# Kernel optimization log

Measured on AMD Instinct MI355X. Metric: run time of the kernel, lower is better.

The kernel has to match this reference:

```python
import jax, jax.numpy as jnp
import numpy as np

# dims: P patches, D=N_azi*N_ele directions, R=P*D radiances, E COO edges,
# T echogram samples, F rfft bins
P, D, R, E, T, NOBJ = 128, 128, 16384, 131072, 1024, 8
F = T // 2 + 1
SR, C_SOUND = 16000.0, 343.0
LOG_GAMMA = float(np.log(1e-3))   # fsm_gamma = 0.001
AIR = 1e-3                        # air absorption coefficient
BOUNCES = 4                       # truncated num_bounces


def setup_inputs():
    key = jax.random.key(0)
    ks = jax.random.split(key, 11)
    return {
        "source_pos": jax.random.normal(ks[0], (3,), jnp.float32) * 2.0,
        "receiver_pos": jax.random.normal(ks[1], (3,), jnp.float32) * 2.0,
        "absorption": jax.random.uniform(ks[2], (NOBJ,), jnp.float32, minval=0.05, maxval=0.6),
        "scattering": jax.random.uniform(ks[3], (NOBJ,), jnp.float32, minval=0.1, maxval=0.9),
        "gk_val": jax.random.uniform(ks[4], (E,), jnp.float32) * 0.1,            # form factors
        "local_kernel_basis": jax.random.uniform(ks[5], (2, D, D), jnp.float32) / D,  # [brdf,Dout,Din]
        "average_distance": jax.random.uniform(ks[6], (R,), jnp.float32) * 10.0 + 1.0,  # meters
        "radiance_pos": jax.random.normal(ks[7], (R, 3), jnp.float32) * 5.0,
        "gk_row": jax.random.randint(ks[8], (E,), 0, R),
        "gk_col": jax.random.randint(ks[9], (E,), 0, R),
        "object_ids": jax.random.randint(ks[10], (P,), 0, NOBJ),
    }


def _path_factor(dist):
    """Frequency-domain factor for a propagation path of length dist [N] -> [N,F].
    Combines fractional delay phase, FSM exponential window gamma^(tau_sec),
    and air absorption exp(-alpha*dist)."""
    freqs = jnp.arange(F, dtype=jnp.float32)
    tau = dist * (SR / C_SOUND)  # delay in samples
    phase = jnp.exp((-2j * np.pi / T) * tau[:, None] * freqs[None, :])
    decay = jnp.exp((LOG_GAMMA / C_SOUND - AIR) * dist)  # fsm + air, per path
    return phase * decay[:, None].astype(phase.dtype)


def reference(source_pos, receiver_pos, absorption, scattering, gk_val,
              local_kernel_basis, average_distance, radiance_pos,
              gk_row, gk_col, object_ids):
    # --- injection: source -> patch-direction radiance [R,F] ---
    d_src = jnp.linalg.norm(radiance_pos - source_pos[None, :], axis=-1)
    g_src = 1.0 / (d_src * d_src + 1e-3)
    rad = g_src[:, None] * _path_factor(d_src)  # complex [R,F]

    # --- BRDF-factorized local kernel: K[p] = sum_b c[b,p] * B[b] ---
    refl = 1.0 - absorption                                   # [NOBJ]
    coeff = jnp.stack([refl * scattering, refl * (1.0 - scattering)])  # [2,NOBJ]
    c_patch = coeff[:, object_ids]                            # [2,P]
    K = jnp.einsum('bp,bde->pde', c_patch, local_kernel_basis)  # [P,Dout,Din]

    prop = _path_factor(average_distance)  # per-radiance transport delay/decay [R,F]

    def bounce(r):
        r = r.reshape(P, D, F)
        r = jnp.einsum('pde,pef->pdf', K.astype(jnp.complex64), r)  # local direction mixing
        r = r.reshape(R, F) * prop
        # sparse COO global kernel: out[row] += val * r[col]
        return jax.ops.segment_sum(gk_val[:, None] * r[gk_col], gk_row, num_segments=R)

    total = rad
    r = rad
    for _ in range(BOUNCES):
        r = bounce(r)
        total = total + r

    # --- detection: patch-direction radiance -> receiver echogram ---
    d_rec = jnp.linalg.norm(radiance_pos - receiver_pos[None, :], axis=-1)
    w_rec = 1.0 / (d_rec * d_rec + 1e-3)
    echo_f = jnp.sum(w_rec[:, None] * _path_factor(d_rec) * total, axis=0)  # [F]

    # FSM correction: divide out the exponential window in time domain
    t = jnp.arange(T, dtype=jnp.float32) / SR
    fsm_window = jnp.exp(LOG_GAMMA * t)
    echogram = jnp.fft.irfft(echo_f, n=T) / fsm_window
    return echogram
```

## Files before the change

kernel.cpp:

```cpp
#include <hip/hip_runtime.h>
#include <math.h>

#define PP 128
#define DD 128
#define RR 16384
#define EE 131072
#define TT 1024
#define FF 513
#define FP 520
#define FPW 528
#define FPITCH 1056
#define NRB 1024
#define PSTRIDE 528
#define EPITCH 136

#define TAU_SCALE 46.64723032069971
#define KDECAY   -0.0211392282f
#define LOG_GAMMA -6.907755278982137f
#define TWO_PI    6.283185307179586

typedef __attribute__((ext_vector_type(8))) short bf16x8;
typedef __attribute__((ext_vector_type(4))) float f32x4;
typedef unsigned short u16;

__device__ __forceinline__ u16 f2bf(float x) {
    unsigned u = __float_as_uint(x);
    unsigned r = (u + 0x7fffu + ((u >> 16) & 1u)) >> 16;
    return (u16)r;
}
__device__ __forceinline__ float bf2f(u16 b) {
    return __uint_as_float(((unsigned)b) << 16);
}

__device__ __forceinline__ void pf_sincos(float tau, int f, float* s, float* c) {
    int ti = (int)tau;
    float tf = tau - (float)ti;
    int m = (ti * f) & 1023;
    float u = fmaf(tf, (float)f, (float)m);
    float ang = u * -0.006135923151542565f;
    __sincosf(ang, s, c);
}

__global__ void k_per_row(const float* __restrict__ rpos,
                          const float* __restrict__ spos,
                          const float* __restrict__ cpos,
                          const float* __restrict__ avg_dist,
                          float* __restrict__ per_row) {
    int r = blockIdx.x * blockDim.x + threadIdx.x;
    if (r >= RR) return;
    float x = rpos[3*r], y = rpos[3*r+1], z = rpos[3*r+2];

    float dx = x - spos[0], dy = y - spos[1], dz = z - spos[2];
    float ds = sqrtf(dx*dx + dy*dy + dz*dz);
    per_row[0*RR + r] = (1.0f/(ds*ds + 0.001f)) * expf(KDECAY * ds);
    per_row[1*RR + r] = ds * (float)TAU_SCALE;

    dx = x - cpos[0]; dy = y - cpos[1]; dz = z - cpos[2];
    float dr = sqrtf(dx*dx + dy*dy + dz*dz);
    per_row[2*RR + r] = (1.0f/(dr*dr + 0.001f)) * expf(KDECAY * dr);
    per_row[3*RR + r] = dr * (float)TAU_SCALE;

    float da = avg_dist[r];
    per_row[4*RR + r] = expf(KDECAY * da);
    per_row[5*RR + r] = da * (float)TAU_SCALE;
}

__global__ void k_build_K(const float* __restrict__ absorption,
                          const float* __restrict__ scattering,
                          const int* __restrict__ object_ids,
                          const float* __restrict__ basis,
                          float* __restrict__ Kmat) {
    int idx = blockIdx.x * 256 + threadIdx.x;
    int p  = idx >> 14;
    int de = idx & 16383;
    int obj = object_ids[p];
    float refl = 1.0f - absorption[obj];
    float sc   = scattering[obj];
    Kmat[idx] = refl*sc*basis[de] + refl*(1.0f - sc)*basis[16384 + de];
}

__global__ void k_count(const int* __restrict__ gk_row, int* __restrict__ counts) {
    int e = blockIdx.x * 256 + threadIdx.x;
    atomicAdd(&counts[gk_row[e]], 1);
}

__global__ __launch_bounds__(1024) void k_scan(const int* __restrict__ counts,
                                               int* __restrict__ row_start,
                                               int* __restrict__ cursor) {
    __shared__ int sh[1024];
    int tid = threadIdx.x;
    int base = tid * 16;
    int local[16];
    int sum = 0;
    #pragma unroll
    for (int j = 0; j < 16; j++) { local[j] = sum; sum += counts[base + j]; }
    sh[tid] = sum;
    __syncthreads();
    for (int off = 1; off < 1024; off <<= 1) {
        int v = (tid >= off) ? sh[tid - off] : 0;
        __syncthreads();
        sh[tid] += v;
        __syncthreads();
    }
    int chunk_excl = sh[tid] - sum;
    #pragma unroll
    for (int j = 0; j < 16; j++) {
        int v = chunk_excl + local[j];
        row_start[base + j] = v;
        cursor[base + j] = v;
    }
    if (tid == 1023) row_start[RR] = chunk_excl + sum;
}

__global__ void k_scatter(const int* __restrict__ gk_row,
                          const float* __restrict__ gk_val,
                          const int* __restrict__ gk_col,
                          int* __restrict__ cursor,
                          int2* __restrict__ edge) {
    int e = blockIdx.x * 256 + threadIdx.x;
    int pos = atomicAdd(&cursor[gk_row[e]], 1);
    edge[pos] = make_int2(gk_col[e], __float_as_int(gk_val[e]));
}

__global__ __launch_bounds__(256) void k_init(const float* __restrict__ per_row,
                                              u16* __restrict__ cur,
                                              float* __restrict__ echo) {
    __shared__ float2 sh[4][64][9];
    int fl = threadIdx.x & 63, rg = threadIdx.x >> 6;
    int r0 = blockIdx.x * 32;
    float2 eacc[9];
    #pragma unroll
    for (int k = 0; k < 9; k++) eacc[k] = make_float2(0.f, 0.f);

    for (int i = 0; i < 8; i++) {
        int r = r0 + rg + i * 4;
        float amp = per_row[r],      tau  = per_row[RR + r];
        float w   = per_row[2*RR+r], taur = per_row[3*RR + r];
        float s1, c1, rs1, rc1, s2, c2, rs2, rc2;
        pf_sincos(tau,  fl, &s1, &c1);  pf_sincos(tau,  64, &rs1, &rc1);
        pf_sincos(taur, fl, &s2, &c2);  pf_sincos(taur, 64, &rs2, &rc2);
        u16* wrow = cur + (size_t)r * FPITCH;
        #pragma unroll
        for (int k = 0; k < 9; k++) {
            int f = fl + (k << 6);
            float re = amp * c1, im = amp * s1;
            if (f < FPW)
                *(unsigned*)(wrow + f * 2) =
                    (unsigned)f2bf(re) | ((unsigned)f2bf(im) << 16);
            if (f < FF) {
                eacc[k].x = fmaf(w, c2*re - s2*im, eacc[k].x);
                eacc[k].y = fmaf(w, c2*im + s2*re, eacc[k].y);
            }
            float n1c = c1*rc1 - s1*rs1, n1s = s1*rc1 + c1*rs1;
            c1 = n1c; s1 = n1s;
            float n2c = c2*rc2 - s2*rs2, n2s = s2*rc2 + c2*rs2;
            c2 = n2c; s2 = n2s;
        }
    }
    #pragma unroll
    for (int k = 0; k < 9; k++) sh[rg][fl][k] = eacc[k];
    __syncthreads();
    if (rg == 0) {
        #pragma unroll
        for (int k = 0; k < 9; k++) {
            int f = fl + (k << 6);
            if (f < FF) {
                float sx = sh[0][fl][k].x + sh[1][fl][k].x + sh[2][fl][k].x + sh[3][fl][k].x;
                float sy = sh[0][fl][k].y + sh[1][fl][k].y + sh[2][fl][k].y + sh[3][fl][k].y;
                atomicAdd(&echo[2*f],   sx);
                atomicAdd(&echo[2*f+1], sy);
            }
        }
    }
}

__global__ __launch_bounds__(256) void k_matmul(const float* __restrict__ Kmat,
                                                const u16* __restrict__ in,
                                                const float* __restrict__ per_row,
                                                u16* __restrict__ out) {
    __shared__ u16 relds[2][16 * EPITCH];
    __shared__ u16 imlds[2][16 * EPITCH];
    int b = blockIdx.x;
    int xcd = b & 7;
    int g = b >> 3;
    int p = (g >> 3) * 8 + xcd;
    int q = g & 7;
    int ct0 = q * 4;
    int ctEnd = (q == 7) ? 33 : ct0 + 4;

    int tid  = threadIdx.x;
    int wave = tid >> 6;
    int lane = tid & 63;
    int quad = lane >> 4;
    int n    = lane & 15;
    int mt0  = wave << 1;

    bf16x8 Ah[2][4], Al[2][4];
    #pragma unroll
    for (int mi = 0; mi < 2; mi++) {
        const float* kp = Kmat + (p << 14) + ((mt0 + mi) * 16 + n) * 128 + quad * 8;
        #pragma unroll
        for (int kt = 0; kt < 4; kt++) {
            float4 x0 = *(const float4*)(kp + kt * 32);
            float4 x1 = *(const float4*)(kp + kt * 32 + 4);
            float xs[8] = {x0.x,x0.y,x0.z,x0.w,x1.x,x1.y,x1.z,x1.w};
            bf16x8 h, l;
            #pragma unroll
            for (int j = 0; j < 8; j++) {
                u16 hb = f2bf(xs[j]);
                h[j] = (short)hb;
                l[j] = (short)f2bf(xs[j] - bf2f(hb));
            }
            Ah[mi][kt] = h; Al[mi][kt] = l;
        }
    }
    float dec_[2][4];
    float pc[2][4], ps[2][4];
    float rc[2][4], rs[2][4];
    #pragma unroll
    for (int mi = 0; mi < 2; mi++)
        #pragma unroll
        for (int r = 0; r < 4; r++) {
            int row = (p << 7) + (mt0 + mi) * 16 + quad * 4 + r;
            dec_[mi][r] = per_row[4*RR + row];
            float tau = per_row[5*RR + row];
            pf_sincos(tau, ct0 * 16 + n, &ps[mi][r], &pc[mi][r]);
            pf_sincos(tau, 16, &rs[mi][r], &rc[mi][r]);
        }

    const u16* pin = in + (size_t)(p << 7) * FPITCH;
    uint4 pk0, pk1;
    int se = tid >> 1, h = tid & 1;
    auto loadTile = [&](int ct) {
        const u16* src = pin + (size_t)se * FPITCH + ct * 32 + h * 16;
        pk0 = *(const uint4*)(src);
        pk1 = *(const uint4*)(src + 8);
    };
    auto writeTile = [&](int buf) {
        unsigned w[8] = {pk0.x, pk0.y, pk0.z, pk0.w, pk1.x, pk1.y, pk1.z, pk1.w};
        int cbase = h * 8;
        #pragma unroll
        for (int k = 0; k < 8; k++) {
            int col = cbase + k;
            relds[buf][col * EPITCH + se] = (u16)(w[k] & 0xffffu);
            imlds[buf][col * EPITCH + se] = (u16)(w[k] >> 16);
        }
    };

    loadTile(ct0); writeTile(0);
    for (int ct = ct0; ct < ctEnd; ct++) {
        int cb = (ct - ct0) & 1;
        __syncthreads();
        if (ct + 1 < ctEnd) { loadTile(ct + 1); writeTile(cb ^ 1); }

        f32x4 ar0 = {0.f,0.f,0.f,0.f}, ar1 = {0.f,0.f,0.f,0.f};
        f32x4 ai0 = {0.f,0.f,0.f,0.f}, ai1 = {0.f,0.f,0.f,0.f};
        const u16* vr = &relds[cb][n * EPITCH];
        const u16* vi = &imlds[cb][n * EPITCH];
        #pragma unroll
        for (int kt = 0; kt < 4; kt++) {
            bf16x8 Br = *(const bf16x8*)(vr + kt * 32 + quad * 8);
            bf16x8 Bi = *(const bf16x8*)(vi + kt * 32 + quad * 8);
            ar0 = __builtin_amdgcn_mfma_f32_16x16x32_bf16(Ah[0][kt], Br, ar0, 0,0,0);
            ar1 = __builtin_amdgcn_mfma_f32_16x16x32_bf16(Ah[1][kt], Br, ar1, 0,0,0);
            ai0 = __builtin_amdgcn_mfma_f32_16x16x32_bf16(Ah[0][kt], Bi, ai0, 0,0,0);
            ai1 = __builtin_amdgcn_mfma_f32_16x16x32_bf16(Ah[1][kt], Bi, ai1, 0,0,0);
            ar0 = __builtin_amdgcn_mfma_f32_16x16x32_bf16(Al[0][kt], Br, ar0, 0,0,0);
            ar1 = __builtin_amdgcn_mfma_f32_16x16x32_bf16(Al[1][kt], Br, ar1, 0,0,0);
            ai0 = __builtin_amdgcn_mfma_f32_16x16x32_bf16(Al[0][kt], Bi, ai0, 0,0,0);
            ai1 = __builtin_amdgcn_mfma_f32_16x16x32_bf16(Al[1][kt], Bi, ai1, 0,0,0);
        }

        int f = ct * 16 + n;
        #pragma unroll
        for (int mi = 0; mi < 2; mi++) {
            f32x4 are = mi ? ar1 : ar0;
            f32x4 aim = mi ? ai1 : ai0;
            #pragma unroll
            for (int r = 0; r < 4; r++) {
                float re = are[r], im = aim[r];
                float s = ps[mi][r], c = pc[mi][r];
                float ore = dec_[mi][r] * (c*re - s*im);
                float oim = dec_[mi][r] * (c*im + s*re);
                int row = (p << 7) + (mt0 + mi) * 16 + quad * 4 + r;
                *(unsigned*)(out + (size_t)row * FPITCH + f * 2) =
                    (unsigned)f2bf(ore) | ((unsigned)f2bf(oim) << 16);
                float nc = c*rc[mi][r] - s*rs[mi][r];
                float nsv = s*rc[mi][r] + c*rs[mi][r];
                pc[mi][r] = nc; ps[mi][r] = nsv;
            }
        }
    }
}

__global__ __launch_bounds__(512) void k_segsum(const int* __restrict__ row_start,
                                                const int2* __restrict__ edge,
                                                const u16* __restrict__ in,
                                                u16* __restrict__ outp,
                                                const float* __restrict__ per_row,
                                                float2* __restrict__ part,
                                                int store_cur) {
    __shared__ float2 sh[4][128][5];
    int rb = blockIdx.x;
    int fl = threadIdx.x & 127, ry = threadIdx.x >> 7;
    bool tail = (fl < 8);
    float2 e0 = {0.f,0.f}, e1 = {0.f,0.f}, e2 = {0.f,0.f}, e3 = {0.f,0.f}, e4 = {0.f,0.f};

    for (int i = 0; i < 4; i++) {
        int row = (rb << 4) + (ry << 2) + i;
        int s0 = row_start[row], s1 = row_start[row + 1];
        float a0r=0.f,a0i=0.f,a1r=0.f,a1i=0.f,a2r=0.f,a2i=0.f,a3r=0.f,a3i=0.f;
        float t4r=0.f,t4i=0.f;
        int t = s0;
        for (; t + 1 < s1; t += 2) {
            int2 ed0 = edge[t], ed1 = edge[t+1];
            float v0 = __int_as_float(ed0.y), v1 = __int_as_float(ed1.y);
            const u16* g0p = in + (size_t)ed0.x * FPITCH + (fl << 1);
            const u16* g1p = in + (size_t)ed1.x * FPITCH + (fl << 1);
            unsigned b00 = *(const unsigned*)(g0p);
            unsigned b01 = *(const unsigned*)(g0p + 256);
            unsigned b02 = *(const unsigned*)(g0p + 512);
            unsigned b03 = *(const unsigned*)(g0p + 768);
            unsigned b10 = *(const unsigned*)(g1p);
            unsigned b11 = *(const unsigned*)(g1p + 256);
            unsigned b12 = *(const unsigned*)(g1p + 512);
            unsigned b13 = *(const unsigned*)(g1p + 768);
            a0r = fmaf(v0, bf2f((u16)(b00 & 0xffffu)), a0r); a0i = fmaf(v0, bf2f((u16)(b00 >> 16)), a0i);
            a1r = fmaf(v0, bf2f((u16)(b01 & 0xffffu)), a1r); a1i = fmaf(v0, bf2f((u16)(b01 >> 16)), a1i);
            a2r = fmaf(v0, bf2f((u16)(b02 & 0xffffu)), a2r); a2i = fmaf(v0, bf2f((u16)(b02 >> 16)), a2i);
            a3r = fmaf(v0, bf2f((u16)(b03 & 0xffffu)), a3r); a3i = fmaf(v0, bf2f((u16)(b03 >> 16)), a3i);
            a0r = fmaf(v1, bf2f((u16)(b10 & 0xffffu)), a0r); a0i = fmaf(v1, bf2f((u16)(b10 >> 16)), a0i);
            a1r = fmaf(v1, bf2f((u16)(b11 & 0xffffu)), a1r); a1i = fmaf(v1, bf2f((u16)(b11 >> 16)), a1i);
            a2r = fmaf(v1, bf2f((u16)(b12 & 0xffffu)), a2r); a2i = fmaf(v1, bf2f((u16)(b12 >> 16)), a2i);
            a3r = fmaf(v1, bf2f((u16)(b13 & 0xffffu)), a3r); a3i = fmaf(v1, bf2f((u16)(b13 >> 16)), a3i);
            if (tail) {
                unsigned b04 = *(const unsigned*)(g0p + 1024);
                unsigned b14 = *(const unsigned*)(g1p + 1024);
                t4r = fmaf(v0, bf2f((u16)(b04 & 0xffffu)), t4r); t4i = fmaf(v0, bf2f((u16)(b04 >> 16)), t4i);
                t4r = fmaf(v1, bf2f((u16)(b14 & 0xffffu)), t4r); t4i = fmaf(v1, bf2f((u16)(b14 >> 16)), t4i);
            }
        }
        if (t < s1) {
            int2 ed = edge[t];
            float v = __int_as_float(ed.y);
            const u16* g = in + (size_t)ed.x * FPITCH + (fl << 1);
            unsigned b0 = *(const unsigned*)(g);
            unsigned b1 = *(const unsigned*)(g + 256);
            unsigned b2 = *(const unsigned*)(g + 512);
            unsigned b3 = *(const unsigned*)(g + 768);
            a0r = fmaf(v, bf2f((u16)(b0 & 0xffffu)), a0r); a0i = fmaf(v, bf2f((u16)(b0 >> 16)), a0i);
            a1r = fmaf(v, bf2f((u16)(b1 & 0xffffu)), a1r); a1i = fmaf(v, bf2f((u16)(b1 >> 16)), a1i);
            a2r = fmaf(v, bf2f((u16)(b2 & 0xffffu)), a2r); a2i = fmaf(v, bf2f((u16)(b2 >> 16)), a2i);
            a3r = fmaf(v, bf2f((u16)(b3 & 0xffffu)), a3r); a3i = fmaf(v, bf2f((u16)(b3 >> 16)), a3i);
            if (tail) {
                unsigned b4 = *(const unsigned*)(g + 1024);
                t4r = fmaf(v, bf2f((u16)(b4 & 0xffffu)), t4r); t4i = fmaf(v, bf2f((u16)(b4 >> 16)), t4i);
            }
        }
        if (store_cur) {
            u16* w = outp + (size_t)row * FPITCH + (fl << 1);
            *(unsigned*)(w)       = (unsigned)f2bf(a0r) | ((unsigned)f2bf(a0i) << 16);
            *(unsigned*)(w + 256) = (unsigned)f2bf(a1r) | ((unsigned)f2bf(a1i) << 16);
            *(unsigned*)(w + 512) = (unsigned)f2bf(a2r) | ((unsigned)f2bf(a2i) << 16);
            *(unsigned*)(w + 768) = (unsigned)f2bf(a3r) | ((unsigned)f2bf(a3i) << 16);
            if (tail)
                *(unsigned*)(w + 1024) = (unsigned)f2bf(t4r) | ((unsigned)f2bf(t4i) << 16);
        }
        float wr = per_row[2*RR + row], taur = per_row[3*RR + row];
        float s, c;
        pf_sincos(taur, fl, &s, &c);
        e0.x = fmaf(wr, c*a0r - s*a0i, e0.x); e0.y = fmaf(wr, c*a0i + s*a0r, e0.y);
        pf_sincos(taur, fl + 128, &s, &c);
        e1.x = fmaf(wr, c*a1r - s*a1i, e1.x); e1.y = fmaf(wr, c*a1i + s*a1r, e1.y);
        pf_sincos(taur, fl + 256, &s, &c);
        e2.x = fmaf(wr, c*a2r - s*a2i, e2.x); e2.y = fmaf(wr, c*a2i + s*a2r, e2.y);
        pf_sincos(taur, fl + 384, &s, &c);
        e3.x = fmaf(wr, c*a3r - s*a3i, e3.x); e3.y = fmaf(wr, c*a3i + s*a3r, e3.y);
        if (tail && (512 + fl) < FF) {
            pf_sincos(taur, 512 + fl, &s, &c);
            e4.x = fmaf(wr, c*t4r - s*t4i, e4.x); e4.y = fmaf(wr, c*t4i + s*t4r, e4.y);
        }
    }
    sh[ry][fl][0] = e0; sh[ry][fl][1] = e1; sh[ry][fl][2] = e2;
    sh[ry][fl][3] = e3; sh[ry][fl][4] = e4;
    __syncthreads();
    if (ry == 0) {
        float2* pp = part + (size_t)rb * PSTRIDE;
        #pragma unroll
        for (int sidx = 0; sidx < 5; sidx++) {
            int fidx = sidx * 128 + fl;
            if (fidx < FP) {
                float2 v0 = sh[0][fl][sidx], v1 = sh[1][fl][sidx];
                float2 v2 = sh[2][fl][sidx], v3 = sh[3][fl][sidx];
                float2 acc = pp[fidx];
                acc.x += v0.x + v1.x + v2.x + v3.x;
                acc.y += v0.y + v1.y + v2.y + v3.y;
                pp[fidx] = acc;
            }
        }
    }
}

__global__ __launch_bounds__(256) void k_fold(const float2* __restrict__ part,
                                              float* __restrict__ echo) {
    int f = blockIdx.x;
    float sx = 0.f, sy = 0.f;
    for (int rb = threadIdx.x; rb < NRB; rb += 256) {
        float2 v = part[(size_t)rb * PSTRIDE + f];
        sx += v.x; sy += v.y;
    }
    for (int off = 32; off >= 1; off >>= 1) {
        sx += __shfl_down(sx, off, 64);
        sy += __shfl_down(sy, off, 64);
    }
    __shared__ float red[2][4];
    int lane = threadIdx.x & 63, w = threadIdx.x >> 6;
    if (lane == 0) { red[0][w] = sx; red[1][w] = sy; }
    __syncthreads();
    if (threadIdx.x == 0) {
        sx = red[0][0]+red[0][1]+red[0][2]+red[0][3];
        sy = red[1][0]+red[1][1]+red[1][2]+red[1][3];
        echo[2*f] += sx;
        echo[2*f+1] += sy;
    }
}

__global__ void k_irfft(const float* __restrict__ echo, float* __restrict__ out) {
    int t = blockIdx.x * blockDim.x + threadIdx.x;
    float acc = echo[0];
    float nyq = echo[2 * 512];
    acc += (t & 1) ? -nyq : nyq;
    for (int f = 1; f < 512; f++) {
        int m = (f * t) & 1023;
        float ang = (float)m * 0.006135923151542565f;
        float s, c; __sincosf(ang, &s, &c);
        acc += 2.0f * (echo[2*f]*c - echo[2*f+1]*s);
    }
    acc *= (1.0f / 1024.0f);
    float tsec = (float)t * (1.0f / 16000.0f);
    float win = expf(LOG_GAMMA * tsec);
    out[t] = acc / win;
}

extern "C" void kernel_launch(void* const* d_in, const int* in_sizes, int n_in,
                              void* d_out, int out_size, void* d_ws, size_t ws_size,
                              hipStream_t stream) {
    const float* source_pos   = (const float*)d_in[0];
    const float* receiver_pos = (const float*)d_in[1];
    const float* absorption   = (const float*)d_in[2];
    const float* scattering   = (const float*)d_in[3];
    const float* gk_val       = (const float*)d_in[4];
    const float* basis        = (const float*)d_in[5];
    const float* avg_dist     = (const float*)d_in[6];
    const float* rpos         = (const float*)d_in[7];
    const int*   gk_row       = (const int*)d_in[8];
    const int*   gk_col       = (const int*)d_in[9];
    const int*   object_ids   = (const int*)d_in[10];
    float* out = (float*)d_out;

    char* base = (char*)d_ws;
    size_t off = 0;
    auto alloc = [&](size_t bytes) -> void* {
        void* ptr = base + off;
        off = (off + bytes + 255) & ~(size_t)255;
        return ptr;
    };
    const size_t PLANE = (size_t)RR * FPITCH + FPITCH;
    float*  Kmat      = (float*)alloc(sizeof(float) * PP * DD * DD);
    u16*    cur       = (u16*)alloc(sizeof(u16) * PLANE);
    u16*    nxt       = (u16*)alloc(sizeof(u16) * PLANE);
    float*  per_row   = (float*)alloc(sizeof(float) * 6 * RR);
    int*    counts    = (int*)alloc(sizeof(int) * RR);
    int*    row_start = (int*)alloc(sizeof(int) * (RR + 1));
    int*    cursor    = (int*)alloc(sizeof(int) * RR);
    int2*   edge      = (int2*)alloc(sizeof(int2) * EE);
    float2* part      = (float2*)alloc(sizeof(float2) * NRB * PSTRIDE);
    float*  echo      = (float*)alloc(sizeof(float) * 1056);

    hipMemsetAsync(counts, 0, sizeof(int) * RR, stream);
    hipMemsetAsync(echo, 0, sizeof(float) * 1056, stream);
    hipMemsetAsync(part, 0, sizeof(float2) * NRB * PSTRIDE, stream);

    k_per_row<<<RR / 256, 256, 0, stream>>>(rpos, source_pos, receiver_pos, avg_dist, per_row);
    k_build_K<<<(PP * DD * DD) / 256, 256, 0, stream>>>(absorption, scattering, object_ids, basis, Kmat);
    k_count<<<EE / 256, 256, 0, stream>>>(gk_row, counts);
    k_scan<<<1, 1024, 0, stream>>>(counts, row_start, cursor);
    k_scatter<<<EE / 256, 256, 0, stream>>>(gk_row, gk_val, gk_col, cursor, edge);
    k_init<<<512, 256, 0, stream>>>(per_row, cur, echo);

    for (int b = 0; b < 4; b++) {
        k_matmul<<<1024, 256, 0, stream>>>(Kmat, cur, per_row, nxt);
        k_segsum<<<NRB, 512, 0, stream>>>(row_start, edge, nxt, cur,
                                          per_row, part, (b < 3) ? 1 : 0);
    }

    k_fold<<<FF, 256, 0, stream>>>(part, echo);
    k_irfft<<<4, 256, 0, stream>>>(echo, out);
}
```

Before: 477.9 us.

## Fuse setup kernels, precompute bf16 hi/lo K split, merge memsets

Merges the per-row geometry, K construction and edge counting kernels into one launch with block-range dispatch. K is now stored as two pre-split bf16 planes (hi and lo), computed once during setup rather than converted from fp32 in every matmul launch. The three memsets become one contiguous memset, which relies on the workspace allocation order (part, echo, counts) being adjacent. The goal is fewer launches and less per-bounce conversion work and K read bandwidth, in exchange for a dependence on that buffer layout.

```diff
diff --git a/kernel.cpp b/kernel.cpp
--- a/kernel.cpp
+++ b/kernel.cpp
@@ -41,47 +41,48 @@
     __sincosf(ang, s, c);
 }
 
-__global__ void k_per_row(const float* __restrict__ rpos,
-                          const float* __restrict__ spos,
-                          const float* __restrict__ cpos,
-                          const float* __restrict__ avg_dist,
-                          float* __restrict__ per_row) {
-    int r = blockIdx.x * blockDim.x + threadIdx.x;
-    if (r >= RR) return;
-    float x = rpos[3*r], y = rpos[3*r+1], z = rpos[3*r+2];
-
-    float dx = x - spos[0], dy = y - spos[1], dz = z - spos[2];
-    float ds = sqrtf(dx*dx + dy*dy + dz*dz);
-    per_row[0*RR + r] = (1.0f/(ds*ds + 0.001f)) * expf(KDECAY * ds);
-    per_row[1*RR + r] = ds * (float)TAU_SCALE;
-
-    dx = x - cpos[0]; dy = y - cpos[1]; dz = z - cpos[2];
-    float dr = sqrtf(dx*dx + dy*dy + dz*dz);
-    per_row[2*RR + r] = (1.0f/(dr*dr + 0.001f)) * expf(KDECAY * dr);
-    per_row[3*RR + r] = dr * (float)TAU_SCALE;
-
-    float da = avg_dist[r];
-    per_row[4*RR + r] = expf(KDECAY * da);
-    per_row[5*RR + r] = da * (float)TAU_SCALE;
-}
-
-__global__ void k_build_K(const float* __restrict__ absorption,
-                          const float* __restrict__ scattering,
-                          const int* __restrict__ object_ids,
-                          const float* __restrict__ basis,
-                          float* __restrict__ Kmat) {
-    int idx = blockIdx.x * 256 + threadIdx.x;
-    int p  = idx >> 14;
-    int de = idx & 16383;
-    int obj = object_ids[p];
-    float refl = 1.0f - absorption[obj];
-    float sc   = scattering[obj];
-    Kmat[idx] = refl*sc*basis[de] + refl*(1.0f - sc)*basis[16384 + de];
-}
-
-__global__ void k_count(const int* __restrict__ gk_row, int* __restrict__ counts) {
-    int e = blockIdx.x * 256 + threadIdx.x;
-    atomicAdd(&counts[gk_row[e]], 1);
+__global__ void k_setup(const float* __restrict__ rpos,
+                        const float* __restrict__ spos,
+                        const float* __restrict__ cpos,
+                        const float* __restrict__ avg_dist,
+                        float* __restrict__ per_row,
+                        const float* __restrict__ absorption,
+                        const float* __restrict__ scattering,
+                        const int* __restrict__ object_ids,
+                        const float* __restrict__ basis,
+                        u16* __restrict__ Kh, u16* __restrict__ Kl,
+                        const int* __restrict__ gk_row,
+                        int* __restrict__ counts) {
+    int b = blockIdx.x;
+    if (b < 8192) {
+        int idx = b * 256 + threadIdx.x;
+        int p  = idx >> 14;
+        int de = idx & 16383;
+        int obj = object_ids[p];
+        float refl = 1.0f - absorption[obj];
+        float sc   = scattering[obj];
+        float kv = refl*sc*basis[de] + refl*(1.0f - sc)*basis[16384 + de];
+        u16 hb = f2bf(kv);
+        Kh[idx] = hb;
+        Kl[idx] = f2bf(kv - bf2f(hb));
+    } else if (b < 8256) {
+        int r = (b - 8192) * 256 + threadIdx.x;
+        float x = rpos[3*r], y = rpos[3*r+1], z = rpos[3*r+2];
+        float dx = x - spos[0], dy = y - spos[1], dz = z - spos[2];
+        float ds = sqrtf(dx*dx + dy*dy + dz*dz);
+        per_row[0*RR + r] = (1.0f/(ds*ds + 0.001f)) * expf(KDECAY * ds);
+        per_row[1*RR + r] = ds * (float)TAU_SCALE;
+        dx = x - cpos[0]; dy = y - cpos[1]; dz = z - cpos[2];
+        float dr = sqrtf(dx*dx + dy*dy + dz*dz);
+        per_row[2*RR + r] = (1.0f/(dr*dr + 0.001f)) * expf(KDECAY * dr);
+        per_row[3*RR + r] = dr * (float)TAU_SCALE;
+        float da = avg_dist[r];
+        per_row[4*RR + r] = expf(KDECAY * da);
+        per_row[5*RR + r] = da * (float)TAU_SCALE;
+    } else {
+        int e = (b - 8256) * 256 + threadIdx.x;
+        atomicAdd(&counts[gk_row[e]], 1);
+    }
 }
 
 __global__ __launch_bounds__(1024) void k_scan(const int* __restrict__ counts,
@@ -174,7 +175,8 @@
     }
 }
 
-__global__ __launch_bounds__(256) void k_matmul(const float* __restrict__ Kmat,
+__global__ __launch_bounds__(256) void k_matmul(const u16* __restrict__ Kh,
+                                                const u16* __restrict__ Kl,
                                                 const u16* __restrict__ in,
                                                 const float* __restrict__ per_row,
                                                 u16* __restrict__ out) {
@@ -198,20 +200,11 @@
     bf16x8 Ah[2][4], Al[2][4];
     #pragma unroll
     for (int mi = 0; mi < 2; mi++) {
-        const float* kp = Kmat + (p << 14) + ((mt0 + mi) * 16 + n) * 128 + quad * 8;
+        size_t rowoff = (size_t)(p << 14) + ((mt0 + mi) * 16 + n) * 128 + quad * 8;
         #pragma unroll
         for (int kt = 0; kt < 4; kt++) {
-            float4 x0 = *(const float4*)(kp + kt * 32);
-            float4 x1 = *(const float4*)(kp + kt * 32 + 4);
-            float xs[8] = {x0.x,x0.y,x0.z,x0.w,x1.x,x1.y,x1.z,x1.w};
-            bf16x8 h, l;
-            #pragma unroll
-            for (int j = 0; j < 8; j++) {
-                u16 hb = f2bf(xs[j]);
-                h[j] = (short)hb;
-                l[j] = (short)f2bf(xs[j] - bf2f(hb));
-            }
-            Ah[mi][kt] = h; Al[mi][kt] = l;
+            Ah[mi][kt] = *(const bf16x8*)(Kh + rowoff + kt * 32);
+            Al[mi][kt] = *(const bf16x8*)(Kl + rowoff + kt * 32);
         }
     }
     float dec_[2][4];
@@ -466,30 +459,30 @@
         return ptr;
     };
     const size_t PLANE = (size_t)RR * FPITCH + FPITCH;
-    float*  Kmat      = (float*)alloc(sizeof(float) * PP * DD * DD);
+    u16*    Kh        = (u16*)alloc(sizeof(u16) * PP * DD * DD);
+    u16*    Kl        = (u16*)alloc(sizeof(u16) * PP * DD * DD);
     u16*    cur       = (u16*)alloc(sizeof(u16) * PLANE);
     u16*    nxt       = (u16*)alloc(sizeof(u16) * PLANE);
     float*  per_row   = (float*)alloc(sizeof(float) * 6 * RR);
-    int*    counts    = (int*)alloc(sizeof(int) * RR);
     int*    row_start = (int*)alloc(sizeof(int) * (RR + 1));
     int*    cursor    = (int*)alloc(sizeof(int) * RR);
     int2*   edge      = (int2*)alloc(sizeof(int2) * EE);
     float2* part      = (float2*)alloc(sizeof(float2) * NRB * PSTRIDE);
     float*  echo      = (float*)alloc(sizeof(float) * 1056);
-
-    hipMemsetAsync(counts, 0, sizeof(int) * RR, stream);
-    hipMemsetAsync(echo, 0, sizeof(float) * 1056, stream);
-    hipMemsetAsync(part, 0, sizeof(float2) * NRB * PSTRIDE, stream);
-
-    k_per_row<<<RR / 256, 256, 0, stream>>>(rpos, source_pos, receiver_pos, avg_dist, per_row);
-    k_build_K<<<(PP * DD * DD) / 256, 256, 0, stream>>>(absorption, scattering, object_ids, basis, Kmat);
-    k_count<<<EE / 256, 256, 0, stream>>>(gk_row, counts);
+    int*    counts    = (int*)alloc(sizeof(int) * RR);
+    size_t  zspan     = (size_t)((char*)(counts + RR) - (char*)part);
+
+    hipMemsetAsync(part, 0, zspan, stream);
+
+    k_setup<<<8768, 256, 0, stream>>>(rpos, source_pos, receiver_pos, avg_dist,
+                                      per_row, absorption, scattering,
+                                      object_ids, basis, Kh, Kl, gk_row, counts);
     k_scan<<<1, 1024, 0, stream>>>(counts, row_start, cursor);
     k_scatter<<<EE / 256, 256, 0, stream>>>(gk_row, gk_val, gk_col, cursor, edge);
     k_init<<<512, 256, 0, stream>>>(per_row, cur, echo);
 
     for (int b = 0; b < 4; b++) {
-        k_matmul<<<1024, 256, 0, stream>>>(Kmat, cur, per_row, nxt);
+        k_matmul<<<1024, 256, 0, stream>>>(Kh, Kl, cur, per_row, nxt);
         k_segsum<<<NRB, 512, 0, stream>>>(row_start, edge, nxt, cur,
                                           per_row, part, (b < 3) ? 1 : 0);
     }
```

Result: faster. 463.9 us (-2.9%).
